# Kernel tuning notes

Hardware: AMD Instinct MI355X
Metric: run time of the kernel (lower is better)

Reference implementation:

```python
import jax, jax.numpy as jnp
import numpy as np

H = 8
D_MODEL = 512
D_K = D_MODEL // H
MAX_REL = 16
BS, LQ, LK = 2, 2048, 2048


def setup_inputs() -> dict:
    key = jax.random.key(0)
    ks = jax.random.split(key, 12)
    s = 0.02
    return {
        'q': jax.random.normal(ks[0], (BS, LQ, D_MODEL), jnp.float32),
        'k': jax.random.normal(ks[1], (BS, LK, D_MODEL), jnp.float32),
        'v': jax.random.normal(ks[2], (BS, LK, D_MODEL), jnp.float32),
        'mask': jnp.ones((BS, LQ, LK), jnp.int32),
        'Wq': jax.random.normal(ks[3], (D_MODEL, D_MODEL), jnp.float32) * s,
        'bq': jnp.zeros((D_MODEL,), jnp.float32),
        'Wk': jax.random.normal(ks[4], (D_MODEL, D_MODEL), jnp.float32) * s,
        'bk': jnp.zeros((D_MODEL,), jnp.float32),
        'Wv': jax.random.normal(ks[5], (D_MODEL, D_MODEL), jnp.float32) * s,
        'bv': jnp.zeros((D_MODEL,), jnp.float32),
        'Wo': jax.random.normal(ks[6], (D_MODEL, D_MODEL), jnp.float32) * s,
        'bo': jnp.zeros((D_MODEL,), jnp.float32),
        'rpe_k': jax.random.normal(ks[7], (2 * MAX_REL + 1, D_K), jnp.float32) * s,
    }


def reference(q, k, v, mask, Wq, bq, Wk, bk, Wv, bv, Wo, bo, rpe_k):
    bs, lq, _ = q.shape
    lk = k.shape[1]
    # projections -> [bs, h, len, d_k]
    qp = (q @ Wq + bq).reshape(bs, lq, H, D_K).transpose(0, 2, 1, 3)
    kp = (k @ Wk + bk).reshape(bs, lk, H, D_K).transpose(0, 2, 1, 3)
    vp = (v @ Wv + bv).reshape(bs, lk, H, D_K).transpose(0, 2, 1, 3)
    content = jnp.einsum('bhqd,bhkd->bhqk', qp, kp)
    # relative position embeddings: [lq, lk, d_k]
    dist = jnp.clip(jnp.arange(lk)[None, :] - jnp.arange(lq)[:, None], -MAX_REL, MAX_REL) + MAX_REL
    rpe = rpe_k[dist]
    rel = jnp.einsum('bhqd,qkd->bhqk', qp, rpe)
    scores = (content + rel) / jnp.sqrt(jnp.asarray(D_K, q.dtype))
    scores = jnp.where(mask[:, None, :, :] == 0, jnp.asarray(-1e9, q.dtype), scores)
    attn = jax.nn.softmax(scores, axis=-1)  # dropout inactive (eval)
    out = jnp.einsum('bhqk,bhkd->bhqd', attn, vp)
    concat = out.transpose(0, 2, 1, 3).reshape(bs, lq, D_MODEL)
    final = concat @ Wo + bo
    return (final, attn)
```

## Files before the change

kernel.cpp:

```cpp
#include <hip/hip_runtime.h>

#define H_ 8
#define DK 64
#define LQ 2048
#define LK 2048
#define BS 2
#define DM 512

typedef _Float16 f16;
typedef _Float16 f16x8 __attribute__((ext_vector_type(8)));
typedef float f32x4 __attribute__((ext_vector_type(4)));
typedef unsigned long long u64;

#define LS 72
#define PS 40
#define RS 48

#define QSCALE 0.1803368801111204f

__global__ __launch_bounds__(256) void prep_k(const int* __restrict__ mask,
                                              u64* __restrict__ mp64,
                                              const float* __restrict__ Wq,
                                              const float* __restrict__ Wk,
                                              const float* __restrict__ Wv,
                                              const float* __restrict__ Wo,
                                              f16* __restrict__ WT,
                                              const float* __restrict__ rpe,
                                              f16* __restrict__ rpef) {
  __shared__ f16 T[64][LS];
  const int bid = blockIdx.x, tid = threadIdx.x;
  if (bid < 32768) {
    size_t t = (size_t)bid * 256 + tid;
    u64 b = __ballot(mask[t] != 0);
    if ((tid & 63) == 0) mp64[t >> 6] = b;
    return;
  }
  if (bid == 33024) {
#pragma unroll
    for (int j = 0; j < 12; j++) {
      int idx = tid + j * 256;
      int row = idx >> 6, d = idx & 63;
      rpef[idx] = row < 33 ? (f16)rpe[row * DK + d] : (f16)0.f;
    }
    return;
  }
  const int idx = bid - 32768;
  const int z = idx >> 6, rem = idx & 63;
  const float* W = z == 0 ? Wq : (z == 1 ? Wk : (z == 2 ? Wv : Wo));
  const int n0 = (rem & 7) * 64, k0 = (rem >> 3) * 64;
  const int r = tid >> 2, cg = tid & 3;
#pragma unroll
  for (int p = 0; p < 4; p++) {
    f32x4 v = *(const f32x4*)(W + (size_t)(k0 + r) * DM + n0 + cg * 16 + p * 4);
#pragma unroll
    for (int j = 0; j < 4; j++) T[cg * 16 + p * 4 + j][r] = (f16)v[j];
  }
  __syncthreads();
  const int n = tid >> 2, kc = tid & 3;
#pragma unroll
  for (int p = 0; p < 2; p++) {
    *(f16x8*)(WT + ((size_t)z * DM + n0 + n) * DM + k0 + kc * 16 + p * 8) =
        *(const f16x8*)&T[n][kc * 16 + p * 8];
  }
}

__global__ __launch_bounds__(256, 4) void qkv_k(
    const float* __restrict__ qin, const float* __restrict__ kin, const float* __restrict__ vin,
    const f16* __restrict__ WT, const f16* __restrict__ rpef,
    const float* __restrict__ bq, const float* __restrict__ bk, const float* __restrict__ bv,
    f16* __restrict__ qp, f16* __restrict__ kp, f16* __restrict__ vpt,
    float* __restrict__ R) {
  __shared__ f16 As[64][LS];
  __shared__ f16 Bt[64][LS];
  const int tid = threadIdx.x, lane = tid & 63, w = tid >> 6;
  const int wr = w >> 1, wc = w & 1, fr = lane & 15, fs = lane >> 4;
  const int m0 = blockIdx.x * 64;
  const int n0g = blockIdx.y * 64, seg = n0g >> 9, nn0 = n0g & 511;
  const float* X = seg == 0 ? qin : (seg == 1 ? kin : vin);
  const f16* WTs = WT + (size_t)seg * DM * DM;
  const float* bias = seg == 0 ? bq : (seg == 1 ? bk : bv);
  const float scale = seg == 0 ? QSCALE : 1.0f;

  f32x4 acc[2][2] = {};

  for (int k0 = 0; k0 < DM; k0 += 64) {
    __syncthreads();
    {
      int m = tid >> 2, c0 = tid & 3;
#pragma unroll
      for (int pp = 0; pp < 2; pp++) {
        int cc = c0 + pp * 4;
        const float* p = X + (size_t)(m0 + m) * DM + k0 + cc * 8;
        f32x4 v0 = *(const f32x4*)p;
        f32x4 v1 = *(const f32x4*)(p + 4);
        f16x8 hv;
#pragma unroll
        for (int i = 0; i < 4; i++) { hv[i] = (f16)v0[i]; hv[i + 4] = (f16)v1[i]; }
        *(f16x8*)&As[m][cc * 8] = hv;
      }
      int n = tid >> 2, kc = tid & 3;
#pragma unroll
      for (int pp = 0; pp < 2; pp++) {
        *(f16x8*)&Bt[n][kc * 16 + pp * 8] =
            *(const f16x8*)(WTs + (size_t)(nn0 + n) * DM + k0 + kc * 16 + pp * 8);
      }
    }
    __syncthreads();
#pragma unroll
    for (int kc = 0; kc < 2; kc++) {
      f16x8 a[2], b[2];
#pragma unroll
      for (int mi = 0; mi < 2; mi++)
        a[mi] = *(const f16x8*)&As[wr * 32 + mi * 16 + fr][kc * 32 + fs * 8];
#pragma unroll
      for (int ni = 0; ni < 2; ni++)
        b[ni] = *(const f16x8*)&Bt[wc * 32 + ni * 16 + fr][kc * 32 + fs * 8];
#pragma unroll
      for (int mi = 0; mi < 2; mi++)
#pragma unroll
        for (int ni = 0; ni < 2; ni++)
          acc[mi][ni] = __builtin_amdgcn_mfma_f32_16x16x32_f16(a[mi], b[ni], acc[mi][ni], 0, 0, 0);
    }
  }

  const int h = nn0 >> 6, b_ = m0 >> 11, l0 = m0 & (LQ - 1);
  if (seg < 2) {
    f16* out = seg == 0 ? qp : kp;
    if (seg == 0) __syncthreads();
#pragma unroll
    for (int mi = 0; mi < 2; mi++)
#pragma unroll
      for (int ni = 0; ni < 2; ni++) {
        int d = wc * 32 + ni * 16 + fr;
        float bb = bias[nn0 + d];
#pragma unroll
        for (int i = 0; i < 4; i++) {
          int row = wr * 32 + mi * 16 + fs * 4 + i;
          f16 hv = (f16)((acc[mi][ni][i] + bb) * scale);
          out[((size_t)(b_ * H_ + h) * LQ + l0 + row) * DK + d] = hv;
          if (seg == 0) As[row][d] = hv;
        }
      }
    if (seg == 0) {
      __syncthreads();
      f16x8 a0 = *(const f16x8*)&As[w * 16 + fr][fs * 8];
      f16x8 a1 = *(const f16x8*)&As[w * 16 + fr][32 + fs * 8];
      const size_t rbase = ((size_t)(b_ * H_ + h) * LQ + l0 + w * 16);
#pragma unroll
      for (int nt = 0; nt < 3; nt++) {
        f16x8 b0 = *(const f16x8*)(rpef + (size_t)(nt * 16 + fr) * DK + fs * 8);
        f16x8 b1 = *(const f16x8*)(rpef + (size_t)(nt * 16 + fr) * DK + 32 + fs * 8);
        f32x4 rc = {};
        rc = __builtin_amdgcn_mfma_f32_16x16x32_f16(a0, b0, rc, 0, 0, 0);
        rc = __builtin_amdgcn_mfma_f32_16x16x32_f16(a1, b1, rc, 0, 0, 0);
#pragma unroll
        for (int i = 0; i < 4; i++)
          R[(rbase + fs * 4 + i) * RS + nt * 16 + fr] = rc[i];
      }
    }
  } else {
    __syncthreads();
#pragma unroll
    for (int mi = 0; mi < 2; mi++)
#pragma unroll
      for (int ni = 0; ni < 2; ni++) {
        int d = wc * 32 + ni * 16 + fr;
        float bb = bias[nn0 + d];
#pragma unroll
        for (int i = 0; i < 4; i++) {
          int ml = wr * 32 + mi * 16 + fs * 4 + i;
          As[d][ml] = (f16)(acc[mi][ni][i] + bb);
        }
      }
    __syncthreads();
    int r = tid >> 2;
#pragma unroll
    for (int pp = 0; pp < 2; pp++) {
      int c = (tid & 3) + pp * 4;
      *(f16x8*)(vpt + ((size_t)((b_ * H_ + h) * DK + r)) * LK + l0 + c * 8) =
          *(const f16x8*)&As[r][c * 8];
    }
  }
}

__global__ __launch_bounds__(512, 4) void attn_k(const f16* __restrict__ qp,
                                                 const f16* __restrict__ kp,
                                                 const f16* __restrict__ vpt,
                                                 const float* __restrict__ R,
                                                 const unsigned* __restrict__ mp,
                                                 float* __restrict__ attn,
                                                 f16* __restrict__ concat) {
  __shared__ f16 Ks[64][LS];
  __shared__ f16 Vt[64][LS];
  __shared__ f16 Pl[8][16][PS];
  __shared__ float Rl[64][34];
  __shared__ float Ph[2][64];
  __shared__ float Oc[4][16][68];
  const int tid = threadIdx.x, lane = tid & 63, w = tid >> 6;
  const int wq = w & 3, wh = w >> 2;
  const int fr = lane & 15, fs = lane >> 4;
  const int flat = blockIdx.x;
  const int idx = flat >> 3;
  const int bh = (flat & 7) * 2 + (idx >> 5), q0 = (idx & 31) * 64;
  const int b = bh >> 3, h = bh & 7;
  const f16* Qb = qp + ((size_t)bh * LQ + q0) * DK;
  const f16* Kb = kp + (size_t)bh * LQ * DK;
  const f16* Vb = vpt + (size_t)bh * DK * LK;

  for (int i2 = tid; i2 < 64 * 34; i2 += 512)
    Rl[i2 / 34][i2 % 34] = R[((size_t)bh * LQ + q0 + i2 / 34) * RS + i2 % 34];
  __syncthreads();

  f16x8 qa[2];
#pragma unroll
  for (int h2 = 0; h2 < 2; h2++)
    qa[h2] = *(const f16x8*)(Qb + (size_t)(wq * 16 + fr) * DK + h2 * 32 + fs * 8);

  int qq[4];
  float rlo[4], rhi[4];
  const unsigned* mprow[4];
#pragma unroll
  for (int i = 0; i < 4; i++) {
    qq[i] = wq * 16 + fs * 4 + i;
    rlo[i] = Rl[qq[i]][0];
    rhi[i] = Rl[qq[i]][32];
    mprow[i] = mp + ((size_t)b * LQ + q0 + qq[i]) * 64;
  }

  float psum[4] = {0.f, 0.f, 0.f, 0.f};
  for (int kt = 0; kt < LK; kt += 64) {
    __syncthreads();
    {
      int r = tid >> 3, c = tid & 7;
      *(f16x8*)&Ks[r][c * 8] = *(const f16x8*)(Kb + (size_t)(kt + r) * DK + c * 8);
    }
    __syncthreads();
    f32x4 sv[2];
#pragma unroll
    for (int cbh = 0; cbh < 2; cbh++) {
      int cb = wh * 2 + cbh;
      f32x4 s = {};
#pragma unroll
      for (int h2 = 0; h2 < 2; h2++) {
        f16x8 bf = *(const f16x8*)&Ks[cb * 16 + fr][h2 * 32 + fs * 8];
        s = __builtin_amdgcn_mfma_f32_16x16x32_f16(qa[h2], bf, s, 0, 0, 0);
      }
      sv[cbh] = s;
    }
    unsigned mw[4];
#pragma unroll
    for (int i = 0; i < 4; i++) mw[i] = mprow[i][(kt >> 5) + wh];
    const int dt = kt - q0;
    if (dt <= -128 || dt >= 128) {
#pragma unroll
      for (int cbh = 0; cbh < 2; cbh++)
#pragma unroll
        for (int i = 0; i < 4; i++) {
          float sc = sv[cbh][i] + (dt < 0 ? rlo[i] : rhi[i]);
          float pv = ((mw[i] >> (cbh * 16 + fr)) & 1u) ? exp2f(sc) : 0.f;
          psum[i] += pv;
        }
    } else {
#pragma unroll
      for (int cbh = 0; cbh < 2; cbh++)
#pragma unroll
        for (int i = 0; i < 4; i++) {
          int dd = dt + wh * 32 + cbh * 16 + fr - qq[i];
          dd = dd < -16 ? -16 : (dd > 16 ? 16 : dd);
          float sc = sv[cbh][i] + Rl[qq[i]][dd + 16];
          float pv = ((mw[i] >> (cbh * 16 + fr)) & 1u) ? exp2f(sc) : 0.f;
          psum[i] += pv;
        }
    }
  }
#pragma unroll
  for (int i = 0; i < 4; i++) {
    float v = psum[i];
    v += __shfl_xor(v, 1);
    v += __shfl_xor(v, 2);
    v += __shfl_xor(v, 4);
    v += __shfl_xor(v, 8);
    psum[i] = v;
  }
  if (fr == 0)
#pragma unroll
    for (int i = 0; i < 4; i++) Ph[wh][qq[i]] = psum[i];
  __syncthreads();
  float inv[4];
#pragma unroll
  for (int i = 0; i < 4; i++) inv[i] = 1.f / (Ph[0][qq[i]] + Ph[1][qq[i]]);

  f32x4 oacc[4] = {};
  for (int kt = 0; kt < LK; kt += 64) {
    __syncthreads();
    {
      int r = tid >> 3, c = tid & 7;
      *(f16x8*)&Ks[r][c * 8] = *(const f16x8*)(Kb + (size_t)(kt + r) * DK + c * 8);
      *(f16x8*)&Vt[r][c * 8] = *(const f16x8*)(Vb + (size_t)r * LK + kt + c * 8);
    }
    __syncthreads();
    f32x4 sv[2];
#pragma unroll
    for (int cbh = 0; cbh < 2; cbh++) {
      int cb = wh * 2 + cbh;
      f32x4 s = {};
#pragma unroll
      for (int h2 = 0; h2 < 2; h2++) {
        f16x8 bf = *(const f16x8*)&Ks[cb * 16 + fr][h2 * 32 + fs * 8];
        s = __builtin_amdgcn_mfma_f32_16x16x32_f16(qa[h2], bf, s, 0, 0, 0);
      }
      sv[cbh] = s;
    }
    unsigned mw[4];
#pragma unroll
    for (int i = 0; i < 4; i++) mw[i] = mprow[i][(kt >> 5) + wh];
    const int dt = kt - q0;
    if (dt <= -128 || dt >= 128) {
#pragma unroll
      for (int cbh = 0; cbh < 2; cbh++)
#pragma unroll
        for (int i = 0; i < 4; i++) {
          float sc = sv[cbh][i] + (dt < 0 ? rlo[i] : rhi[i]);
          float pv = ((mw[i] >> (cbh * 16 + fr)) & 1u) ? exp2f(sc) * inv[i] : 0.f;
          Pl[w][fs * 4 + i][cbh * 16 + fr] = (f16)pv;
        }
    } else {
#pragma unroll
      for (int cbh = 0; cbh < 2; cbh++)
#pragma unroll
        for (int i = 0; i < 4; i++) {
          int dd = dt + wh * 32 + cbh * 16 + fr - qq[i];
          dd = dd < -16 ? -16 : (dd > 16 ? 16 : dd);
          float sc = sv[cbh][i] + Rl[qq[i]][dd + 16];
          float pv = ((mw[i] >> (cbh * 16 + fr)) & 1u) ? exp2f(sc) * inv[i] : 0.f;
          Pl[w][fs * 4 + i][cbh * 16 + fr] = (f16)pv;
        }
    }
    {
      f16x8 pa = *(const f16x8*)&Pl[w][fr][fs * 8];
#pragma unroll
      for (int db = 0; db < 4; db++) {
        f16x8 vb = *(const f16x8*)&Vt[db * 16 + fr][wh * 32 + fs * 8];
        oacc[db] = __builtin_amdgcn_mfma_f32_16x16x32_f16(pa, vb, oacc[db], 0, 0, 0);
      }
    }
    {
      int r2 = lane >> 2, cq = lane & 3;
      float* arow = attn + ((size_t)bh * LQ + q0 + wq * 16 + r2) * LK + kt + wh * 32 + cq * 8;
      f16x8 pv8 = *(const f16x8*)&Pl[w][r2][cq * 8];
      f32x4 o0 = {(float)pv8[0], (float)pv8[1], (float)pv8[2], (float)pv8[3]};
      f32x4 o1 = {(float)pv8[4], (float)pv8[5], (float)pv8[6], (float)pv8[7]};
      __builtin_nontemporal_store(o0, (f32x4*)arow);
      __builtin_nontemporal_store(o1, (f32x4*)(arow + 4));
    }
  }

  __syncthreads();
  if (wh == 1) {
#pragma unroll
    for (int db = 0; db < 4; db++)
#pragma unroll
      for (int i = 0; i < 4; i++) Oc[wq][fs * 4 + i][db * 16 + fr] = oacc[db][i];
  }
  __syncthreads();
  if (wh == 0) {
#pragma unroll
    for (int db = 0; db < 4; db++)
#pragma unroll
      for (int i = 0; i < 4; i++) {
        float val = oacc[db][i] + Oc[wq][fs * 4 + i][db * 16 + fr];
        int gq = q0 + wq * 16 + fs * 4 + i;
        concat[((size_t)b * LQ + gq) * DM + h * DK + db * 16 + fr] = (f16)val;
      }
  }
}

__global__ __launch_bounds__(256, 4) void ogemm_k(const f16* __restrict__ X,
                                                  const f16* __restrict__ WT,
                                                  const float* __restrict__ bias,
                                                  float* __restrict__ out) {
  __shared__ f16 As[64][LS];
  __shared__ f16 Bt[64][LS];
  const int tid = threadIdx.x, lane = tid & 63, w = tid >> 6;
  const int wr = w >> 1, wc = w & 1, fr = lane & 15, fs = lane >> 4;
  const int m0 = blockIdx.x * 64, n0 = blockIdx.y * 64;
  const f16* WTo = WT + (size_t)3 * DM * DM;

  f32x4 acc[2][2] = {};
  for (int k0 = 0; k0 < DM; k0 += 64) {
    __syncthreads();
    {
      int r = tid >> 2, c0 = tid & 3;
#pragma unroll
      for (int pp = 0; pp < 2; pp++) {
        int c = c0 + pp * 4;
        *(f16x8*)&As[r][c * 8] = *(const f16x8*)(X + (size_t)(m0 + r) * DM + k0 + c * 8);
      }
      int n = tid >> 2, kc = tid & 3;
#pragma unroll
      for (int pp = 0; pp < 2; pp++) {
        *(f16x8*)&Bt[n][kc * 16 + pp * 8] =
            *(const f16x8*)(WTo + (size_t)(n0 + n) * DM + k0 + kc * 16 + pp * 8);
      }
    }
    __syncthreads();
#pragma unroll
    for (int kc = 0; kc < 2; kc++) {
      f16x8 a[2], b[2];
#pragma unroll
      for (int mi = 0; mi < 2; mi++)
        a[mi] = *(const f16x8*)&As[wr * 32 + mi * 16 + fr][kc * 32 + fs * 8];
#pragma unroll
      for (int ni = 0; ni < 2; ni++)
        b[ni] = *(const f16x8*)&Bt[wc * 32 + ni * 16 + fr][kc * 32 + fs * 8];
#pragma unroll
      for (int mi = 0; mi < 2; mi++)
#pragma unroll
        for (int ni = 0; ni < 2; ni++)
          acc[mi][ni] = __builtin_amdgcn_mfma_f32_16x16x32_f16(a[mi], b[ni], acc[mi][ni], 0, 0, 0);
    }
  }
#pragma unroll
  for (int mi = 0; mi < 2; mi++)
#pragma unroll
    for (int ni = 0; ni < 2; ni++) {
      int gcol = n0 + wc * 32 + ni * 16 + fr;
      float bb = bias[gcol];
#pragma unroll
      for (int i = 0; i < 4; i++) {
        int grow = m0 + wr * 32 + mi * 16 + fs * 4 + i;
        out[(size_t)grow * DM + gcol] = acc[mi][ni][i] + bb;
      }
    }
}

extern "C" void kernel_launch(void* const* d_in, const int* in_sizes, int n_in,
                              void* d_out, int out_size, void* d_ws, size_t ws_size,
                              hipStream_t stream) {
  const float* q = (const float*)d_in[0];
  const float* k = (const float*)d_in[1];
  const float* v = (const float*)d_in[2];
  const int* mask = (const int*)d_in[3];
  const float* Wq = (const float*)d_in[4];
  const float* bq = (const float*)d_in[5];
  const float* Wk = (const float*)d_in[6];
  const float* bk = (const float*)d_in[7];
  const float* Wv = (const float*)d_in[8];
  const float* bv = (const float*)d_in[9];
  const float* Wo = (const float*)d_in[10];
  const float* bo = (const float*)d_in[11];
  const float* rpe = (const float*)d_in[12];

  char* ws = (char*)d_ws;
  f16* qp = (f16*)(ws);
  f16* kp = (f16*)(ws + (1u << 22));
  f16* vpt = (f16*)(ws + (2u << 22));
  float* R = (float*)(ws + (3u << 22));
  size_t off = (3u << 22) + (size_t)32768 * RS * 4;
  u64* mp64 = (u64*)(ws + off);
  f16* concat = (f16*)(ws + off + (1u << 20));
  f16* WT = (f16*)(ws + off + (1u << 20) + (1u << 22));
  f16* rpef = (f16*)(ws + off + (1u << 20) + (1u << 22) + (1u << 21));

  float* final_out = (float*)d_out;
  float* attn_out = final_out + (size_t)BS * LQ * DM;

  prep_k<<<dim3(33025), 256, 0, stream>>>(mask, mp64, Wq, Wk, Wv, Wo, WT, rpe, rpef);

  qkv_k<<<dim3(64, 24), 256, 0, stream>>>(q, k, v, WT, rpef, bq, bk, bv, qp, kp, vpt, R);

  attn_k<<<dim3(512), 512, 0, stream>>>(qp, kp, vpt, R, (const unsigned*)mp64, attn_out,
                                        concat);

  ogemm_k<<<dim3(64, 8), 256, 0, stream>>>(concat, WT, bo, final_out);
}
```

Measured before the change: 163.0 us.

## Transpose QK^T MFMA so P stays in registers, drop LDS P staging

Swaps the MFMA operand order so each lane holds scores for a single query row and four consecutive keys. That output layout can feed the P·V MFMA (16x16x16) directly as the A operand and be written to attn as fp32 without round-tripping through the shared-memory Pl buffer. It also switches to 64-bit mask words per row, simplifies the row-sum reduction to two shuffles, and stores attn probabilities directly in fp32 rather than converting from f16. The trade-off is twice as many smaller MFMAs for P·V, and lane-strided global stores for attn.

```diff
diff --git a/kernel.cpp b/kernel.cpp
--- a/kernel.cpp
+++ b/kernel.cpp
@@ -8,12 +8,12 @@
 #define DM 512
 
 typedef _Float16 f16;
+typedef _Float16 f16x4 __attribute__((ext_vector_type(4)));
 typedef _Float16 f16x8 __attribute__((ext_vector_type(8)));
 typedef float f32x4 __attribute__((ext_vector_type(4)));
 typedef unsigned long long u64;
 
 #define LS 72
-#define PS 40
 #define RS 48
 
 #define QSCALE 0.1803368801111204f
@@ -187,12 +187,11 @@
                                                  const f16* __restrict__ kp,
                                                  const f16* __restrict__ vpt,
                                                  const float* __restrict__ R,
-                                                 const unsigned* __restrict__ mp,
+                                                 const u64* __restrict__ mp64,
                                                  float* __restrict__ attn,
                                                  f16* __restrict__ concat) {
   __shared__ f16 Ks[64][LS];
   __shared__ f16 Vt[64][LS];
-  __shared__ f16 Pl[8][16][PS];
   __shared__ float Rl[64][34];
   __shared__ float Ph[2][64];
   __shared__ float Oc[4][16][68];
@@ -216,18 +215,11 @@
   for (int h2 = 0; h2 < 2; h2++)
     qa[h2] = *(const f16x8*)(Qb + (size_t)(wq * 16 + fr) * DK + h2 * 32 + fs * 8);
 
-  int qq[4];
-  float rlo[4], rhi[4];
-  const unsigned* mprow[4];
-#pragma unroll
-  for (int i = 0; i < 4; i++) {
-    qq[i] = wq * 16 + fs * 4 + i;
-    rlo[i] = Rl[qq[i]][0];
-    rhi[i] = Rl[qq[i]][32];
-    mprow[i] = mp + ((size_t)b * LQ + q0 + qq[i]) * 64;
-  }
-
-  float psum[4] = {0.f, 0.f, 0.f, 0.f};
+  const int qrow = wq * 16 + fr;
+  const float rlo = Rl[qrow][0], rhi = Rl[qrow][32];
+  const u64* mrow = mp64 + ((size_t)b * LQ + q0 + qrow) * 32;
+
+  float psum = 0.f;
   for (int kt = 0; kt < LK; kt += 64) {
     __syncthreads();
     {
@@ -235,60 +227,40 @@
       *(f16x8*)&Ks[r][c * 8] = *(const f16x8*)(Kb + (size_t)(kt + r) * DK + c * 8);
     }
     __syncthreads();
-    f32x4 sv[2];
+    u64 mw = mrow[kt >> 6];
+    const int dt = kt - q0;
 #pragma unroll
     for (int cbh = 0; cbh < 2; cbh++) {
       int cb = wh * 2 + cbh;
       f32x4 s = {};
 #pragma unroll
       for (int h2 = 0; h2 < 2; h2++) {
-        f16x8 bf = *(const f16x8*)&Ks[cb * 16 + fr][h2 * 32 + fs * 8];
-        s = __builtin_amdgcn_mfma_f32_16x16x32_f16(qa[h2], bf, s, 0, 0, 0);
-      }
-      sv[cbh] = s;
-    }
-    unsigned mw[4];
-#pragma unroll
-    for (int i = 0; i < 4; i++) mw[i] = mprow[i][(kt >> 5) + wh];
-    const int dt = kt - q0;
-    if (dt <= -128 || dt >= 128) {
-#pragma unroll
-      for (int cbh = 0; cbh < 2; cbh++)
-#pragma unroll
-        for (int i = 0; i < 4; i++) {
-          float sc = sv[cbh][i] + (dt < 0 ? rlo[i] : rhi[i]);
-          float pv = ((mw[i] >> (cbh * 16 + fr)) & 1u) ? exp2f(sc) : 0.f;
-          psum[i] += pv;
-        }
-    } else {
-#pragma unroll
-      for (int cbh = 0; cbh < 2; cbh++)
-#pragma unroll
-        for (int i = 0; i < 4; i++) {
-          int dd = dt + wh * 32 + cbh * 16 + fr - qq[i];
+        f16x8 kf = *(const f16x8*)&Ks[cb * 16 + fr][h2 * 32 + fs * 8];
+        s = __builtin_amdgcn_mfma_f32_16x16x32_f16(kf, qa[h2], s, 0, 0, 0);
+      }
+      if (dt <= -128 || dt >= 128) {
+        float radd = dt < 0 ? rlo : rhi;
+#pragma unroll
+        for (int i = 0; i < 4; i++) {
+          int kb = wh * 32 + cbh * 16 + fs * 4 + i;
+          psum += ((mw >> kb) & 1ull) ? exp2f(s[i] + radd) : 0.f;
+        }
+      } else {
+#pragma unroll
+        for (int i = 0; i < 4; i++) {
+          int kb = wh * 32 + cbh * 16 + fs * 4 + i;
+          int dd = dt + kb - qrow;
           dd = dd < -16 ? -16 : (dd > 16 ? 16 : dd);
-          float sc = sv[cbh][i] + Rl[qq[i]][dd + 16];
-          float pv = ((mw[i] >> (cbh * 16 + fr)) & 1u) ? exp2f(sc) : 0.f;
-          psum[i] += pv;
-        }
-    }
-  }
-#pragma unroll
-  for (int i = 0; i < 4; i++) {
-    float v = psum[i];
-    v += __shfl_xor(v, 1);
-    v += __shfl_xor(v, 2);
-    v += __shfl_xor(v, 4);
-    v += __shfl_xor(v, 8);
-    psum[i] = v;
-  }
-  if (fr == 0)
-#pragma unroll
-    for (int i = 0; i < 4; i++) Ph[wh][qq[i]] = psum[i];
+          psum += ((mw >> kb) & 1ull) ? exp2f(s[i] + Rl[qrow][dd + 16]) : 0.f;
+        }
+      }
+    }
+  }
+  psum += __shfl_xor(psum, 16);
+  psum += __shfl_xor(psum, 32);
+  if (fs == 0) Ph[wh][qrow] = psum;
   __syncthreads();
-  float inv[4];
-#pragma unroll
-  for (int i = 0; i < 4; i++) inv[i] = 1.f / (Ph[0][qq[i]] + Ph[1][qq[i]]);
+  const float inv = 1.f / (Ph[0][qrow] + Ph[1][qrow]);
 
   f32x4 oacc[4] = {};
   for (int kt = 0; kt < LK; kt += 64) {
@@ -299,59 +271,45 @@
       *(f16x8*)&Vt[r][c * 8] = *(const f16x8*)(Vb + (size_t)r * LK + kt + c * 8);
     }
     __syncthreads();
-    f32x4 sv[2];
+    u64 mw = mrow[kt >> 6];
+    const int dt = kt - q0;
 #pragma unroll
     for (int cbh = 0; cbh < 2; cbh++) {
       int cb = wh * 2 + cbh;
       f32x4 s = {};
 #pragma unroll
       for (int h2 = 0; h2 < 2; h2++) {
-        f16x8 bf = *(const f16x8*)&Ks[cb * 16 + fr][h2 * 32 + fs * 8];
-        s = __builtin_amdgcn_mfma_f32_16x16x32_f16(qa[h2], bf, s, 0, 0, 0);
-      }
-      sv[cbh] = s;
-    }
-    unsigned mw[4];
-#pragma unroll
-    for (int i = 0; i < 4; i++) mw[i] = mprow[i][(kt >> 5) + wh];
-    const int dt = kt - q0;
-    if (dt <= -128 || dt >= 128) {
-#pragma unroll
-      for (int cbh = 0; cbh < 2; cbh++)
-#pragma unroll
-        for (int i = 0; i < 4; i++) {
-          float sc = sv[cbh][i] + (dt < 0 ? rlo[i] : rhi[i]);
-          float pv = ((mw[i] >> (cbh * 16 + fr)) & 1u) ? exp2f(sc) * inv[i] : 0.f;
-          Pl[w][fs * 4 + i][cbh * 16 + fr] = (f16)pv;
-        }
-    } else {
-#pragma unroll
-      for (int cbh = 0; cbh < 2; cbh++)
-#pragma unroll
-        for (int i = 0; i < 4; i++) {
-          int dd = dt + wh * 32 + cbh * 16 + fr - qq[i];
+        f16x8 kf = *(const f16x8*)&Ks[cb * 16 + fr][h2 * 32 + fs * 8];
+        s = __builtin_amdgcn_mfma_f32_16x16x32_f16(kf, qa[h2], s, 0, 0, 0);
+      }
+      f32x4 pvv;
+      if (dt <= -128 || dt >= 128) {
+        float radd = dt < 0 ? rlo : rhi;
+#pragma unroll
+        for (int i = 0; i < 4; i++) {
+          int kb = wh * 32 + cbh * 16 + fs * 4 + i;
+          pvv[i] = ((mw >> kb) & 1ull) ? exp2f(s[i] + radd) * inv : 0.f;
+        }
+      } else {
+#pragma unroll
+        for (int i = 0; i < 4; i++) {
+          int kb = wh * 32 + cbh * 16 + fs * 4 + i;
+          int dd = dt + kb - qrow;
           dd = dd < -16 ? -16 : (dd > 16 ? 16 : dd);
-          float sc = sv[cbh][i] + Rl[qq[i]][dd + 16];
-          float pv = ((mw[i] >> (cbh * 16 + fr)) & 1u) ? exp2f(sc) * inv[i] : 0.f;
-          Pl[w][fs * 4 + i][cbh * 16 + fr] = (f16)pv;
-        }
-    }
-    {
-      f16x8 pa = *(const f16x8*)&Pl[w][fr][fs * 8];
+          pvv[i] = ((mw >> kb) & 1ull) ? exp2f(s[i] + Rl[qrow][dd + 16]) * inv : 0.f;
+        }
+      }
+      __builtin_nontemporal_store(
+          pvv, (f32x4*)(attn + ((size_t)bh * LQ + q0 + qrow) * LK + kt + wh * 32 +
+                        cbh * 16 + fs * 4));
+      f16x4 pa;
+#pragma unroll
+      for (int j = 0; j < 4; j++) pa[j] = (f16)pvv[j];
 #pragma unroll
       for (int db = 0; db < 4; db++) {
-        f16x8 vb = *(const f16x8*)&Vt[db * 16 + fr][wh * 32 + fs * 8];
-        oacc[db] = __builtin_amdgcn_mfma_f32_16x16x32_f16(pa, vb, oacc[db], 0, 0, 0);
-      }
-    }
-    {
-      int r2 = lane >> 2, cq = lane & 3;
-      float* arow = attn + ((size_t)bh * LQ + q0 + wq * 16 + r2) * LK + kt + wh * 32 + cq * 8;
-      f16x8 pv8 = *(const f16x8*)&Pl[w][r2][cq * 8];
-      f32x4 o0 = {(float)pv8[0], (float)pv8[1], (float)pv8[2], (float)pv8[3]};
-      f32x4 o1 = {(float)pv8[4], (float)pv8[5], (float)pv8[6], (float)pv8[7]};
-      __builtin_nontemporal_store(o0, (f32x4*)arow);
-      __builtin_nontemporal_store(o1, (f32x4*)(arow + 4));
+        f16x4 vb = *(const f16x4*)&Vt[db * 16 + fr][wh * 32 + cbh * 16 + fs * 4];
+        oacc[db] = __builtin_amdgcn_mfma_f32_16x16x16f16(pa, vb, oacc[db], 0, 0, 0);
+      }
     }
   }
 
@@ -469,8 +427,7 @@
 
   qkv_k<<<dim3(64, 24), 256, 0, stream>>>(q, k, v, WT, rpef, bq, bk, bv, qp, kp, vpt, R);
 
-  attn_k<<<dim3(512), 512, 0, stream>>>(qp, kp, vpt, R, (const unsigned*)mp64, attn_out,
-                                        concat);
+  attn_k<<<dim3(512), 512, 0, stream>>>(qp, kp, vpt, R, mp64, attn_out, concat);
 
   ogemm_k<<<dim3(64, 8), 256, 0, stream>>>(concat, WT, bo, final_out);
 }
```

New measurement: 168.4 us. +3.3%, slower.
